# Kernel tuning notes

Measured on AMD Instinct MI355X. Metric: run time of the kernel, lower is better.

The kernel has to match this reference:

```python
import jax, jax.numpy as jnp
import numpy as np

B, S, D = 2, 2048, 1024
H, HD = 16, 64          # num_heads, head_dim = D // H
W = 31                  # window_size (odd)
E = 1024                # embed_dim


def setup_inputs() -> dict:
    key = jax.random.key(0)
    ks = jax.random.split(key, 12)
    sd = 1.0 / np.sqrt(D)
    so = 1.0 / np.sqrt(H * HD)
    return {
        "x": jax.random.normal(ks[0], (B, S, D), jnp.float32),
        "fsq": jax.random.normal(ks[1], (1, S, D), jnp.float32),   # feature_squeeze_token
        "pos": jax.random.normal(ks[2], (1, S, D), jnp.float32),   # position_token
        "Wq": jax.random.normal(ks[3], (H, D, HD), jnp.float32) * sd,
        "bq": jax.random.normal(ks[4], (H, HD), jnp.float32) * sd,
        "Wk": jax.random.normal(ks[5], (H, D, HD), jnp.float32) * sd,
        "bk": jax.random.normal(ks[6], (H, HD), jnp.float32) * sd,
        "Wv": jax.random.normal(ks[7], (H, D, HD), jnp.float32) * sd,
        "bv": jax.random.normal(ks[8], (H, HD), jnp.float32) * sd,
        "Wo": jax.random.normal(ks[9], (H * HD, E), jnp.float32) * so,
        "bo": jax.random.normal(ks[10], (E,), jnp.float32) * so,
    }


def reference(x, fsq, pos, Wq, bq, Wk, bk, Wv, bv, Wo, bo):
    b, s, d = x.shape
    pad = (W - 1) // 2
    # sliding windows: (B, S, W, D), zero-padded at sequence edges
    xp = jnp.pad(x, ((0, 0), (pad, pad), (0, 0)))
    idx = jnp.arange(s)[:, None] + jnp.arange(W)[None, :]  # (S, W)
    win = xp[:, idx, :]  # (B, S, W, D)
    a = jnp.broadcast_to(fsq[:, :, None, :], (b, s, 1, d))  # squeeze token per pos
    bt = jnp.broadcast_to(pos[:, :, None, :], (b, s, 1, d))  # position token per pos
    kv = jnp.concatenate([win, bt, a], axis=2)  # (B, S, K=W+2, D)
    q = jnp.broadcast_to(fsq, (b, s, d))        # query = squeeze token
    # per-head projections (heads stacked on axis h)
    qh = jnp.einsum("bsd,hde->bhse", q, Wq) + bq[None, :, None, :]        # (B,H,S,HD)
    kh = jnp.einsum("bskd,hde->bhske", kv, Wk) + bk[None, :, None, None, :]
    vh = jnp.einsum("bskd,hde->bhske", kv, Wv) + bv[None, :, None, None, :]
    scores = jnp.einsum("bhse,bhske->bhsk", qh, kh) / jnp.sqrt(jnp.asarray(HD, x.dtype))
    attn = jax.nn.softmax(scores, axis=-1)  # dropout is identity in eval
    outh = jnp.einsum("bhsk,bhske->bhse", attn, vh)  # (B,H,S,HD)
    concat = outh.transpose(0, 2, 1, 3).reshape(b, s, H * HD)  # heads concat order 0..H-1
    return concat @ Wo + bo  # (B, S, E)
```

## Files before the change

### kernel.cpp

```cpp
#include <hip/hip_runtime.h>


typedef __attribute__((ext_vector_type(8))) short bf16x8;
typedef __attribute__((ext_vector_type(4))) float f32x4;
typedef unsigned short u16;
typedef unsigned int u32;

__device__ __forceinline__ float bf2f(u16 u) {
  union { u32 i; float f; } v; v.i = ((u32)u) << 16; return v.f;
}
__device__ __forceinline__ u16 f2bf(float f) {
  union { float f; u32 i; } v; v.f = f;
  u32 r = v.i + 0x7fffu + ((v.i >> 16) & 1u);
  return (u16)(r >> 16);
}
__device__ __forceinline__ float2 unpk(u32 u) {
  union { u32 i; float f; } lo, hi;
  lo.i = u << 16; hi.i = u & 0xffff0000u;
  return make_float2(lo.f, hi.f);
}
__device__ __forceinline__ float dot8(uint4 a, uint4 b) {
  float s = 0.f;
  { float2 x = unpk(a.x), y = unpk(b.x); s += x.x*y.x + x.y*y.y; }
  { float2 x = unpk(a.y), y = unpk(b.y); s += x.x*y.x + x.y*y.y; }
  { float2 x = unpk(a.z), y = unpk(b.z); s += x.x*y.x + x.y*y.y; }
  { float2 x = unpk(a.w), y = unpk(b.w); s += x.x*y.x + x.y*y.y; }
  return s;
}
__device__ __forceinline__ void gload_lds16(const u16* g, u16* l) {
  __builtin_amdgcn_global_load_lds((const __attribute__((address_space(1))) void*)(g),
                                   (__attribute__((address_space(3))) void*)(l),
                                   16, 0, 0);
}
__device__ __forceinline__ uint4 pack8(float4 a, float4 b) {
  union { u16 h[8]; uint4 q; } u;
  u.h[0] = f2bf(a.x); u.h[1] = f2bf(a.y); u.h[2] = f2bf(a.z); u.h[3] = f2bf(a.w);
  u.h[4] = f2bf(b.x); u.h[5] = f2bf(b.y); u.h[6] = f2bf(b.z); u.h[7] = f2bf(b.w);
  return u.q;
}

__global__ __launch_bounds__(256) void f2b_all(const float* __restrict__ x,
                                               const float* __restrict__ fsq,
                                               const float* __restrict__ pos,
                                               u16* __restrict__ xb,
                                               u16* __restrict__ fsqb,
                                               u16* __restrict__ posb) {
  int i = blockIdx.x * 256 + threadIdx.x;
  const float* src; u16* dst; int off;
  if (i < 524288)      { src = x;   dst = xb;   off = i; }
  else if (i < 786432) { src = fsq; dst = fsqb; off = i - 524288; }
  else                 { src = pos; dst = posb; off = i - 786432; }
  float4 a = ((const float4*)src)[2 * off];
  float4 b = ((const float4*)src)[2 * off + 1];
  ((uint4*)dst)[off] = pack8(a, b);
}

__device__ __forceinline__ void transpose_body(const float* src, u16* dst,
                                               int R, int C, int r0, int c0) {
  __shared__ u16 tile[64][72];
  int t = threadIdx.x;
#pragma unroll
  for (int i = 0; i < 16; ++i) {
    int idx = i * 256 + t;
    int r = idx >> 6, c = idx & 63;
    tile[r][c] = f2bf(src[(size_t)(r0 + r) * C + (c0 + c)]);
  }
  __syncthreads();
#pragma unroll
  for (int i = 0; i < 16; ++i) {
    int idx = i * 256 + t;
    int c = idx >> 6, r = idx & 63;
    dst[(size_t)(c0 + c) * R + (r0 + r)] = tile[r][c];
  }
}

__global__ __launch_bounds__(256) void transpose_all(const float* __restrict__ Wq,
                                                     const float* __restrict__ Wk,
                                                     const float* __restrict__ Wv,
                                                     const float* __restrict__ Wo,
                                                     u16* __restrict__ WqT,
                                                     u16* __restrict__ WkT,
                                                     u16* __restrict__ WvT,
                                                     u16* __restrict__ WoT) {
  int z = blockIdx.z;
  if (z < 3) {
    const float* s = (z == 0) ? Wq : (z == 1) ? Wk : Wv;
    u16* d = (z == 0) ? WqT : (z == 1) ? WkT : WvT;
    size_t off = (size_t)blockIdx.x * 65536;
    transpose_body(s + off, d + off, 1024, 64, blockIdx.y * 64, 0);
  } else {
    transpose_body(Wo, WoT, 1024, 1024, blockIdx.y * 64, blockIdx.x * 64);
  }
}

__device__ __forceinline__ int swz(int R, int c) {
  return (R * 8 + (c ^ (R & 7))) * 8;
}

template <bool OUTF32>
__device__ __forceinline__ void gemm_body(const u16* __restrict__ Ap,
                                          const u16* __restrict__ BT,
                                          const float* __restrict__ bias,
                                          void* Cp, int tile_n) {
  __shared__ u16 As[128 * 64];
  __shared__ u16 Bs[128 * 64];
  const int t = threadIdx.x, lane = t & 63, wave = t >> 6;
  const int wm = (wave >> 1) * 64, wn = (wave & 1) * 64;
  const int row16 = lane & 15, quad = lane >> 4;
  const int l8 = lane >> 3;
  const int cswz = (lane & 7) ^ l8;

  f32x4 acc[4][4] = {};

  for (int k0 = 0; k0 < 1024; k0 += 64) {
    __syncthreads();
#pragma unroll
    for (int j = 0; j < 4; ++j) {
      int r = wave * 32 + j * 8 + l8;
      gload_lds16(Ap + (size_t)r * 1024 + k0 + cswz * 8,
                  &As[wave * 2048 + j * 512]);
      gload_lds16(BT + (size_t)(tile_n + r) * 1024 + k0 + cswz * 8,
                  &Bs[wave * 2048 + j * 512]);
    }
    __syncthreads();

#pragma unroll
    for (int kb = 0; kb < 2; ++kb) {
      bf16x8 a_frag[4], b_frag[4];
#pragma unroll
      for (int i = 0; i < 4; ++i)
        a_frag[i] = *(const bf16x8*)&As[swz(wm + i * 16 + row16, kb * 4 + quad)];
#pragma unroll
      for (int j = 0; j < 4; ++j)
        b_frag[j] = *(const bf16x8*)&Bs[swz(wn + j * 16 + row16, kb * 4 + quad)];
#pragma unroll
      for (int i = 0; i < 4; ++i)
#pragma unroll
        for (int j = 0; j < 4; ++j)
          acc[i][j] = __builtin_amdgcn_mfma_f32_16x16x32_bf16(
              a_frag[i], b_frag[j], acc[i][j], 0, 0, 0);
    }
  }

#pragma unroll
  for (int j = 0; j < 4; ++j) {
    int n = tile_n + wn + j * 16 + row16;
    float bb = bias[n];
#pragma unroll
    for (int i = 0; i < 4; ++i) {
      int m0 = wm + i * 16 + quad * 4;
#pragma unroll
      for (int r = 0; r < 4; ++r) {
        float val = acc[i][j][r] + bb;
        if (OUTF32) ((float*)Cp)[(size_t)(m0 + r) * 1024 + n] = val;
        else        ((u16*)Cp)[(size_t)(m0 + r) * 1024 + n] = f2bf(val);
      }
    }
  }
}

__global__ __launch_bounds__(256) void proj_gemm(const u16* __restrict__ xb,
                                                 const u16* __restrict__ fsqb,
                                                 const u16* __restrict__ posb,
                                                 const u16* __restrict__ WkT,
                                                 const u16* __restrict__ WvT,
                                                 const u16* __restrict__ WqT,
                                                 const float* __restrict__ bk,
                                                 const float* __restrict__ bv,
                                                 const float* __restrict__ bq,
                                                 u16* __restrict__ Kp,
                                                 u16* __restrict__ Vp,
                                                 u16* __restrict__ Qp) {
  int bid = blockIdx.x;
  const u16* Ap; const u16* BT; const float* bias; u16* C; int tile_n;
  if (bid < 1024) {
    int tm = bid >> 4, tn = bid & 15;
    if (tm < 32)      Ap = xb   + (size_t)tm * 128 * 1024;
    else if (tm < 48) Ap = fsqb + (size_t)(tm - 32) * 128 * 1024;
    else              Ap = posb + (size_t)(tm - 48) * 128 * 1024;
    if (tn < 8) { BT = WkT; bias = bk; C = Kp + (size_t)tm * 128 * 1024; tile_n = tn * 128; }
    else        { BT = WvT; bias = bv; C = Vp + (size_t)tm * 128 * 1024; tile_n = (tn - 8) * 128; }
  } else {
    int q = bid - 1024; int tm = q >> 3; tile_n = (q & 7) * 128;
    Ap = fsqb + (size_t)tm * 128 * 1024; BT = WqT; bias = bq;
    C = Qp + (size_t)tm * 128 * 1024;
  }
  gemm_body<false>(Ap, BT, bias, C, tile_n);
}

__global__ __launch_bounds__(256) void out_gemm(const u16* __restrict__ Att,
                                                const u16* __restrict__ WoT,
                                                const float* __restrict__ bo,
                                                float* __restrict__ Out) {
  int tile_n = blockIdx.x * 128, tm = blockIdx.y;
  gemm_body<true>(Att + (size_t)tm * 128 * 1024, WoT, bo,
                  Out + (size_t)tm * 128 * 1024, tile_n);
}

#define AST 72
#define QS  0
#define KWS 2304
#define VTS 6912
#define KPS 11520
#define PS  20736

__global__ __launch_bounds__(256) void attn_tile(const u16* __restrict__ Qp,
                                                 const u16* __restrict__ Kp,
                                                 const u16* __restrict__ Vp,
                                                 const float* __restrict__ bk,
                                                 const float* __restrict__ bv,
                                                 u16* __restrict__ Att) {
  __shared__ u16 sm[23040];
  __shared__ float smP[32 * 36];

  const int t = threadIdx.x;
  const int bid = blockIdx.x;
  const int s0 = (bid & 63) * 32;
  const int h  = (bid >> 6) & 15;
  const int b  = bid >> 10;
  const int lane = t & 63, wave = t >> 6;
  const int row16 = lane & 15, quad = lane >> 4;
  const int hcol = h * 64;

  { int w = t >> 3, oct = t & 7;
    *(uint4*)&sm[QS + w * AST + oct * 8] =
        *(const uint4*)(Qp + (size_t)(s0 + w) * 1024 + hcol + oct * 8); }
#pragma unroll
  for (int i = 0; i < 2; ++i) {
    int task = i * 256 + t; int w = task >> 3, oct = task & 7;
    int g = s0 + w - 15;
    uint4 v;
    if ((unsigned)g < 2048u)
      v = *(const uint4*)(Kp + (size_t)(b * 2048 + g) * 1024 + hcol + oct * 8);
    else
      v = pack8(*(const float4*)(bk + hcol + oct * 8),
                *(const float4*)(bk + hcol + oct * 8 + 4));
    *(uint4*)&sm[KWS + w * AST + oct * 8] = v;
  }
#pragma unroll
  for (int i = 0; i < 4; ++i) {
    int task = i * 256 + t;
    int which = task >> 8, r = (task >> 3) & 31, oct = task & 7;
    const u16* src = (which < 2) ? Kp : Vp;
    size_t grow = ((which & 1) == 0) ? (size_t)(6144 + s0 + r)
                                     : (size_t)(4096 + s0 + r);
    *(uint4*)&sm[KPS + which * 2304 + r * AST + oct * 8] =
        *(const uint4*)(src + grow * 1024 + hcol + oct * 8);
  }
#pragma unroll
  for (int i = 0; i < 2; ++i) {
    int task = i * 256 + t; int w = task >> 3, oct = task & 7;
    int g = s0 + w - 15;
    union { u16 h8[8]; uint4 q; } u;
    if ((unsigned)g < 2048u)
      u.q = *(const uint4*)(Vp + (size_t)(b * 2048 + g) * 1024 + hcol + oct * 8);
    else
      u.q = pack8(*(const float4*)(bv + hcol + oct * 8),
                  *(const float4*)(bv + hcol + oct * 8 + 4));
#pragma unroll
    for (int j = 0; j < 8; ++j)
      sm[VTS + (oct * 8 + j) * AST + w] = u.h8[j];
  }
  __syncthreads();

  {
    f32x4 accS[2] = {};
#pragma unroll
    for (int kc = 0; kc < 2; ++kc) {
      bf16x8 bf_ = *(const bf16x8*)&sm[KWS + (wave * 16 + row16) * AST + kc * 32 + quad * 8];
#pragma unroll
      for (int mi = 0; mi < 2; ++mi) {
        bf16x8 af = *(const bf16x8*)&sm[QS + (mi * 16 + row16) * AST + kc * 32 + quad * 8];
        accS[mi] = __builtin_amdgcn_mfma_f32_16x16x32_bf16(af, bf_, accS[mi], 0, 0, 0);
      }
    }
#pragma unroll
    for (int mi = 0; mi < 2; ++mi)
#pragma unroll
      for (int r = 0; r < 4; ++r) {
        int s = mi * 16 + quad * 4 + r;
        int w = wave * 16 + row16;
        int d = w - s;
        if (d >= 0 && d <= 30) smP[s * 36 + d] = accS[mi][r] * 0.125f;
      }
  }
  if (t < 64) {
    int s = t >> 1, which = t & 1;
    int base = KPS + which * 2304;
    float a = 0.f;
#pragma unroll
    for (int c = 0; c < 8; ++c)
      a += dot8(*(const uint4*)&sm[QS + s * AST + c * 8],
                *(const uint4*)&sm[base + s * AST + c * 8]);
    smP[s * 36 + 31 + which] = a * 0.125f;
  }
  __syncthreads();

  if (t < 32) {
    int s = t;
    float vals[33];
#pragma unroll
    for (int k = 0; k < 33; ++k) vals[k] = smP[s * 36 + k];
    float mx = -1e30f;
#pragma unroll
    for (int k = 0; k < 33; ++k) mx = fmaxf(mx, vals[k]);
    float sum = 0.f;
#pragma unroll
    for (int k = 0; k < 33; ++k) { vals[k] = __expf(vals[k] - mx); sum += vals[k]; }
    float inv = 1.f / sum;
    u32* prow = (u32*)&sm[PS + s * AST];
#pragma unroll
    for (int j = 0; j < 32; ++j) prow[j] = 0;
#pragma unroll
    for (int k = 0; k < 31; ++k)
      sm[PS + s * AST + s + k] = f2bf(vals[k] * inv);
    smP[s * 36 + 33] = vals[31] * inv;
    smP[s * 36 + 34] = vals[32] * inv;
  }
  __syncthreads();

  {
    f32x4 accO[2] = {};
#pragma unroll
    for (int kc = 0; kc < 2; ++kc) {
      bf16x8 bf_ = *(const bf16x8*)&sm[VTS + (wave * 16 + row16) * AST + kc * 32 + quad * 8];
#pragma unroll
      for (int mi = 0; mi < 2; ++mi) {
        bf16x8 af = *(const bf16x8*)&sm[PS + (mi * 16 + row16) * AST + kc * 32 + quad * 8];
        accO[mi] = __builtin_amdgcn_mfma_f32_16x16x32_bf16(af, bf_, accO[mi], 0, 0, 0);
      }
    }
#pragma unroll
    for (int mi = 0; mi < 2; ++mi)
#pragma unroll
      for (int r = 0; r < 4; ++r) {
        int s = mi * 16 + quad * 4 + r;
        int e = wave * 16 + row16;
        float o = accO[mi][r]
                + smP[s * 36 + 33] * bf2f(sm[KPS + 2 * 2304 + s * AST + e])
                + smP[s * 36 + 34] * bf2f(sm[KPS + 3 * 2304 + s * AST + e]);
        Att[(size_t)(b * 2048 + s0 + s) * 1024 + hcol + e] = f2bf(o);
      }
  }
}

extern "C" void kernel_launch(void* const* d_in, const int* in_sizes, int n_in,
                              void* d_out, int out_size, void* d_ws, size_t ws_size,
                              hipStream_t stream) {
  (void)in_sizes; (void)n_in; (void)out_size; (void)ws_size;

  const float* x   = (const float*)d_in[0];
  const float* fsq = (const float*)d_in[1];
  const float* pos = (const float*)d_in[2];
  const float* Wq  = (const float*)d_in[3];
  const float* bq  = (const float*)d_in[4];
  const float* Wk  = (const float*)d_in[5];
  const float* bk  = (const float*)d_in[6];
  const float* Wv  = (const float*)d_in[7];
  const float* bv  = (const float*)d_in[8];
  const float* Wo  = (const float*)d_in[9];
  const float* bo  = (const float*)d_in[10];

  u16* ws = (u16*)d_ws;
  const size_t M1 = 1024 * 1024;
  u16* WqT  = ws + 0 * M1;
  u16* WkT  = ws + 1 * M1;
  u16* WvT  = ws + 2 * M1;
  u16* WoT  = ws + 3 * M1;
  u16* Qp   = ws + 4 * M1;
  u16* Kp   = ws + 6 * M1;
  u16* Vp   = ws + 14 * M1;
  u16* fsqb = ws + 22 * M1;
  u16* posb = ws + 24 * M1;
  u16* xb   = ws + 26 * M1;
  u16* Att  = ws + 22 * M1;

  f2b_all<<<4096, 256, 0, stream>>>(x, fsq, pos, xb, fsqb, posb);
  transpose_all<<<dim3(16, 16, 4), 256, 0, stream>>>(Wq, Wk, Wv, Wo,
                                                     WqT, WkT, WvT, WoT);

  proj_gemm<<<1152, 256, 0, stream>>>(xb, fsqb, posb, WkT, WvT, WqT,
                                      bk, bv, bq, Kp, Vp, Qp);

  attn_tile<<<2048, 256, 0, stream>>>(Qp, Kp, Vp, bk, bv, Att);

  out_gemm<<<dim3(8, 32), 256, 0, stream>>>(Att, WoT, bo, (float*)d_out);
}
```

Before: 214.0 us.

## Merge prep kernels, halve out_gemm M-tile, shrink attention shared memory

Fuses the fp32-to-bf16 conversion and weight-transpose kernels into one launch to save a launch and its idle gap. Templates the GEMM body on its M-tile so out_gemm uses 64-row tiles, doubling its grid from 256 to 512 blocks to better fill the CUs. Shrinks attention shared memory by reusing the Q buffer for probabilities and reading the two extra V rows straight from global memory, which should allow more resident blocks per CU at the cost of uncoalesced global reads in the epilogue.

```diff
diff --git a/kernel.cpp b/kernel.cpp
--- a/kernel.cpp
+++ b/kernel.cpp
@@ -39,22 +39,6 @@
   return u.q;
 }
 
-__global__ __launch_bounds__(256) void f2b_all(const float* __restrict__ x,
-                                               const float* __restrict__ fsq,
-                                               const float* __restrict__ pos,
-                                               u16* __restrict__ xb,
-                                               u16* __restrict__ fsqb,
-                                               u16* __restrict__ posb) {
-  int i = blockIdx.x * 256 + threadIdx.x;
-  const float* src; u16* dst; int off;
-  if (i < 524288)      { src = x;   dst = xb;   off = i; }
-  else if (i < 786432) { src = fsq; dst = fsqb; off = i - 524288; }
-  else                 { src = pos; dst = posb; off = i - 786432; }
-  float4 a = ((const float4*)src)[2 * off];
-  float4 b = ((const float4*)src)[2 * off + 1];
-  ((uint4*)dst)[off] = pack8(a, b);
-}
-
 __device__ __forceinline__ void transpose_body(const float* src, u16* dst,
                                                int R, int C, int r0, int c0) {
   __shared__ u16 tile[64][72];
@@ -74,22 +58,42 @@
   }
 }
 
-__global__ __launch_bounds__(256) void transpose_all(const float* __restrict__ Wq,
-                                                     const float* __restrict__ Wk,
-                                                     const float* __restrict__ Wv,
-                                                     const float* __restrict__ Wo,
-                                                     u16* __restrict__ WqT,
-                                                     u16* __restrict__ WkT,
-                                                     u16* __restrict__ WvT,
-                                                     u16* __restrict__ WoT) {
-  int z = blockIdx.z;
-  if (z < 3) {
-    const float* s = (z == 0) ? Wq : (z == 1) ? Wk : Wv;
-    u16* d = (z == 0) ? WqT : (z == 1) ? WkT : WvT;
-    size_t off = (size_t)blockIdx.x * 65536;
-    transpose_body(s + off, d + off, 1024, 64, blockIdx.y * 64, 0);
+__global__ __launch_bounds__(256) void prep(const float* __restrict__ x,
+                                            const float* __restrict__ fsq,
+                                            const float* __restrict__ pos,
+                                            const float* __restrict__ Wq,
+                                            const float* __restrict__ Wk,
+                                            const float* __restrict__ Wv,
+                                            const float* __restrict__ Wo,
+                                            u16* __restrict__ xb,
+                                            u16* __restrict__ fsqb,
+                                            u16* __restrict__ posb,
+                                            u16* __restrict__ WqT,
+                                            u16* __restrict__ WkT,
+                                            u16* __restrict__ WvT,
+                                            u16* __restrict__ WoT) {
+  int bid = blockIdx.x;
+  if (bid < 4096) {
+    int i = bid * 256 + threadIdx.x;
+    const float* src; u16* dst; int off;
+    if (i < 524288)      { src = x;   dst = xb;   off = i; }
+    else if (i < 786432) { src = fsq; dst = fsqb; off = i - 524288; }
+    else                 { src = pos; dst = posb; off = i - 786432; }
+    float4 a = ((const float4*)src)[2 * off];
+    float4 b = ((const float4*)src)[2 * off + 1];
+    ((uint4*)dst)[off] = pack8(a, b);
   } else {
-    transpose_body(Wo, WoT, 1024, 1024, blockIdx.y * 64, blockIdx.x * 64);
+    int id = bid - 4096;
+    int z = id >> 8, rest = id & 255;
+    int xx = rest & 15, yy = rest >> 4;
+    if (z < 3) {
+      const float* s = (z == 0) ? Wq : (z == 1) ? Wk : Wv;
+      u16* d = (z == 0) ? WqT : (z == 1) ? WkT : WvT;
+      size_t off = (size_t)xx * 65536;
+      transpose_body(s + off, d + off, 1024, 64, yy * 64, 0);
+    } else {
+      transpose_body(Wo, WoT, 1024, 1024, yy * 64, xx * 64);
+    }
   }
 }
 
@@ -97,28 +101,32 @@
   return (R * 8 + (c ^ (R & 7))) * 8;
 }
 
-template <bool OUTF32>
+template <int MT, bool OUTF32>
 __device__ __forceinline__ void gemm_body(const u16* __restrict__ Ap,
                                           const u16* __restrict__ BT,
                                           const float* __restrict__ bias,
                                           void* Cp, int tile_n) {
-  __shared__ u16 As[128 * 64];
+  __shared__ u16 As[MT * 32 * 64];
   __shared__ u16 Bs[128 * 64];
   const int t = threadIdx.x, lane = t & 63, wave = t >> 6;
-  const int wm = (wave >> 1) * 64, wn = (wave & 1) * 64;
+  const int wm = (wave >> 1) * (MT * 16), wn = (wave & 1) * 64;
   const int row16 = lane & 15, quad = lane >> 4;
   const int l8 = lane >> 3;
   const int cswz = (lane & 7) ^ l8;
 
-  f32x4 acc[4][4] = {};
+  f32x4 acc[MT][4] = {};
 
   for (int k0 = 0; k0 < 1024; k0 += 64) {
     __syncthreads();
 #pragma unroll
+    for (int j = 0; j < MT; ++j) {
+      int r = wave * (MT * 8) + j * 8 + l8;
+      gload_lds16(Ap + (size_t)r * 1024 + k0 + cswz * 8,
+                  &As[wave * (MT * 512) + j * 512]);
+    }
+#pragma unroll
     for (int j = 0; j < 4; ++j) {
       int r = wave * 32 + j * 8 + l8;
-      gload_lds16(Ap + (size_t)r * 1024 + k0 + cswz * 8,
-                  &As[wave * 2048 + j * 512]);
       gload_lds16(BT + (size_t)(tile_n + r) * 1024 + k0 + cswz * 8,
                   &Bs[wave * 2048 + j * 512]);
     }
@@ -126,15 +134,15 @@
 
 #pragma unroll
     for (int kb = 0; kb < 2; ++kb) {
-      bf16x8 a_frag[4], b_frag[4];
-#pragma unroll
-      for (int i = 0; i < 4; ++i)
+      bf16x8 a_frag[MT], b_frag[4];
+#pragma unroll
+      for (int i = 0; i < MT; ++i)
         a_frag[i] = *(const bf16x8*)&As[swz(wm + i * 16 + row16, kb * 4 + quad)];
 #pragma unroll
       for (int j = 0; j < 4; ++j)
         b_frag[j] = *(const bf16x8*)&Bs[swz(wn + j * 16 + row16, kb * 4 + quad)];
 #pragma unroll
-      for (int i = 0; i < 4; ++i)
+      for (int i = 0; i < MT; ++i)
 #pragma unroll
         for (int j = 0; j < 4; ++j)
           acc[i][j] = __builtin_amdgcn_mfma_f32_16x16x32_bf16(
@@ -147,7 +155,7 @@
     int n = tile_n + wn + j * 16 + row16;
     float bb = bias[n];
 #pragma unroll
-    for (int i = 0; i < 4; ++i) {
+    for (int i = 0; i < MT; ++i) {
       int m0 = wm + i * 16 + quad * 4;
 #pragma unroll
       for (int r = 0; r < 4; ++r) {
@@ -185,7 +193,7 @@
     Ap = fsqb + (size_t)tm * 128 * 1024; BT = WqT; bias = bq;
     C = Qp + (size_t)tm * 128 * 1024;
   }
-  gemm_body<false>(Ap, BT, bias, C, tile_n);
+  gemm_body<4, false>(Ap, BT, bias, C, tile_n);
 }
 
 __global__ __launch_bounds__(256) void out_gemm(const u16* __restrict__ Att,
@@ -193,8 +201,8 @@
                                                 const float* __restrict__ bo,
                                                 float* __restrict__ Out) {
   int tile_n = blockIdx.x * 128, tm = blockIdx.y;
-  gemm_body<true>(Att + (size_t)tm * 128 * 1024, WoT, bo,
-                  Out + (size_t)tm * 128 * 1024, tile_n);
+  gemm_body<2, true>(Att + (size_t)tm * 64 * 1024, WoT, bo,
+                     Out + (size_t)tm * 64 * 1024, tile_n);
 }
 
 #define AST 72
@@ -202,7 +210,8 @@
 #define KWS 2304
 #define VTS 6912
 #define KPS 11520
-#define PS  20736
+#define KFS 13824
+#define SMT 16128
 
 __global__ __launch_bounds__(256) void attn_tile(const u16* __restrict__ Qp,
                                                  const u16* __restrict__ Kp,
@@ -210,7 +219,7 @@
                                                  const float* __restrict__ bk,
                                                  const float* __restrict__ bv,
                                                  u16* __restrict__ Att) {
-  __shared__ u16 sm[23040];
+  __shared__ u16 sm[SMT];
   __shared__ float smP[32 * 36];
 
   const int t = threadIdx.x;
@@ -238,14 +247,12 @@
     *(uint4*)&sm[KWS + w * AST + oct * 8] = v;
   }
 #pragma unroll
-  for (int i = 0; i < 4; ++i) {
+  for (int i = 0; i < 2; ++i) {
     int task = i * 256 + t;
-    int which = task >> 8, r = (task >> 3) & 31, oct = task & 7;
-    const u16* src = (which < 2) ? Kp : Vp;
-    size_t grow = ((which & 1) == 0) ? (size_t)(6144 + s0 + r)
-                                     : (size_t)(4096 + s0 + r);
-    *(uint4*)&sm[KPS + which * 2304 + r * AST + oct * 8] =
-        *(const uint4*)(src + grow * 1024 + hcol + oct * 8);
+    int r = (task >> 3) & 31, oct = task & 7;
+    size_t grow = (i == 0) ? (size_t)(6144 + s0 + r) : (size_t)(4096 + s0 + r);
+    *(uint4*)&sm[(i == 0 ? KPS : KFS) + r * AST + oct * 8] =
+        *(const uint4*)(Kp + grow * 1024 + hcol + oct * 8);
   }
 #pragma unroll
   for (int i = 0; i < 2; ++i) {
@@ -286,7 +293,7 @@
   }
   if (t < 64) {
     int s = t >> 1, which = t & 1;
-    int base = KPS + which * 2304;
+    int base = (which == 0) ? KPS : KFS;
     float a = 0.f;
 #pragma unroll
     for (int c = 0; c < 8; ++c)
@@ -308,12 +315,12 @@
 #pragma unroll
     for (int k = 0; k < 33; ++k) { vals[k] = __expf(vals[k] - mx); sum += vals[k]; }
     float inv = 1.f / sum;
-    u32* prow = (u32*)&sm[PS + s * AST];
+    u32* prow = (u32*)&sm[QS + s * AST];
 #pragma unroll
     for (int j = 0; j < 32; ++j) prow[j] = 0;
 #pragma unroll
     for (int k = 0; k < 31; ++k)
-      sm[PS + s * AST + s + k] = f2bf(vals[k] * inv);
+      sm[QS + s * AST + s + k] = f2bf(vals[k] * inv);
     smP[s * 36 + 33] = vals[31] * inv;
     smP[s * 36 + 34] = vals[32] * inv;
   }
@@ -326,7 +333,7 @@
       bf16x8 bf_ = *(const bf16x8*)&sm[VTS + (wave * 16 + row16) * AST + kc * 32 + quad * 8];
 #pragma unroll
       for (int mi = 0; mi < 2; ++mi) {
-        bf16x8 af = *(const bf16x8*)&sm[PS + (mi * 16 + row16) * AST + kc * 32 + quad * 8];
+        bf16x8 af = *(const bf16x8*)&sm[QS + (mi * 16 + row16) * AST + kc * 32 + quad * 8];
         accO[mi] = __builtin_amdgcn_mfma_f32_16x16x32_bf16(af, bf_, accO[mi], 0, 0, 0);
       }
     }
@@ -337,8 +344,8 @@
         int s = mi * 16 + quad * 4 + r;
         int e = wave * 16 + row16;
         float o = accO[mi][r]
-                + smP[s * 36 + 33] * bf2f(sm[KPS + 2 * 2304 + s * AST + e])
-                + smP[s * 36 + 34] * bf2f(sm[KPS + 3 * 2304 + s * AST + e]);
+                + smP[s * 36 + 33] * bf2f(Vp[(size_t)(6144 + s0 + s) * 1024 + hcol + e])
+                + smP[s * 36 + 34] * bf2f(Vp[(size_t)(4096 + s0 + s) * 1024 + hcol + e]);
         Att[(size_t)(b * 2048 + s0 + s) * 1024 + hcol + e] = f2bf(o);
       }
   }
@@ -375,14 +382,13 @@
   u16* xb   = ws + 26 * M1;
   u16* Att  = ws + 22 * M1;
 
-  f2b_all<<<4096, 256, 0, stream>>>(x, fsq, pos, xb, fsqb, posb);
-  transpose_all<<<dim3(16, 16, 4), 256, 0, stream>>>(Wq, Wk, Wv, Wo,
-                                                     WqT, WkT, WvT, WoT);
+  prep<<<5120, 256, 0, stream>>>(x, fsq, pos, Wq, Wk, Wv, Wo,
+                                 xb, fsqb, posb, WqT, WkT, WvT, WoT);
 
   proj_gemm<<<1152, 256, 0, stream>>>(xb, fsqb, posb, WkT, WvT, WqT,
                                       bk, bv, bq, Kp, Vp, Qp);
 
   attn_tile<<<2048, 256, 0, stream>>>(Qp, Kp, Vp, bk, bv, Att);
 
-  out_gemm<<<dim3(8, 32), 256, 0, stream>>>(Att, WoT, bo, (float*)d_out);
-}
+  out_gemm<<<dim3(8, 64), 256, 0, stream>>>(Att, WoT, bo, (float*)d_out);
+}
```

Result: faster. 198.9 us (-7.0%).
